# Optimization experiments

Measured on AMD Instinct MI355X. Metric: run time of the kernel, lower is better.

## Reference

```python
import math
import jax, jax.numpy as jnp
import numpy as np

B, T, N_FEAT, H = 16, 1024, 512, 8
D_K = N_FEAT // H  # 64


def setup_inputs() -> dict:
    key = jax.random.key(0)
    ks = jax.random.split(key, 16)
    s = 0.02
    return {
        "query": jax.random.normal(ks[0], (B, T, N_FEAT), jnp.float32),
        "key": jax.random.normal(ks[1], (B, T, N_FEAT), jnp.float32),
        "value": jax.random.normal(ks[2], (B, T, N_FEAT), jnp.float32),
        "pos_emb": jax.random.normal(ks[3], (1, T, N_FEAT), jnp.float32),
        "mask": jnp.zeros((B, 1, T), jnp.float32),  # additive bias, 0 = attend
        "Wq": jax.random.normal(ks[4], (N_FEAT, N_FEAT), jnp.float32) * s,
        "bq": jnp.zeros((N_FEAT,), jnp.float32),
        "Wk": jax.random.normal(ks[5], (N_FEAT, N_FEAT), jnp.float32) * s,
        "bk": jnp.zeros((N_FEAT,), jnp.float32),
        "Wv": jax.random.normal(ks[6], (N_FEAT, N_FEAT), jnp.float32) * s,
        "bv": jnp.zeros((N_FEAT,), jnp.float32),
        "Wo": jax.random.normal(ks[7], (N_FEAT, N_FEAT), jnp.float32) * s,
        "bo": jnp.zeros((N_FEAT,), jnp.float32),
        "Wpos": jax.random.normal(ks[8], (N_FEAT, N_FEAT), jnp.float32) * s,
        "pos_bias_u": jax.random.normal(ks[9], (H, D_K), jnp.float32) * 0.05,
        "pos_bias_v": jax.random.normal(ks[10], (H, D_K), jnp.float32) * 0.05,
    }


def reference(query, key, value, pos_emb, mask,
              Wq, bq, Wk, bk, Wv, bv, Wo, bo, Wpos,
              pos_bias_u, pos_bias_v):
    b, t, _ = query.shape
    h, d_k = pos_bias_u.shape
    # projections -> head-split
    q = (query @ Wq + bq).reshape(b, t, h, d_k)                 # (B,T,H,D)
    k = (key @ Wk + bk).reshape(b, -1, h, d_k).transpose(0, 2, 1, 3)    # (B,H,S,D)
    v = (value @ Wv + bv).reshape(b, -1, h, d_k).transpose(0, 2, 1, 3)  # (B,H,S,D)
    p = (pos_emb @ Wpos).reshape(pos_emb.shape[1], h, d_k).transpose(1, 0, 2)  # (H,S,D)
    # Transformer-XL content/position biased queries
    q_u = (q + pos_bias_u).transpose(0, 2, 1, 3)  # (B,H,T,D)
    q_v = (q + pos_bias_v).transpose(0, 2, 1, 3)  # (B,H,T,D)
    matrix_ac = jnp.einsum('bhtd,bhsd->bhts', q_u, k)
    matrix_bd = jnp.einsum('bhtd,hsd->bhts', q_v, p)
    scores = (matrix_ac + matrix_bd) / math.sqrt(d_k) + mask[:, None]  # (B,H,T,S)
    attn = jax.nn.softmax(scores, axis=-1)
    out = jnp.einsum('bhts,bhsd->bthd', attn, v).reshape(b, t, h * d_k)
    return out @ Wo + bo  # (B,T,n_feat)
```

## Files before the change

kernel.cpp:

```cpp
#include <hip/hip_runtime.h>

#define BB 16
#define TT 1024
#define HH 8
#define DD 64
#define NF 512

typedef __attribute__((ext_vector_type(4))) float f4;
typedef __attribute__((ext_vector_type(8))) short s8;
typedef __attribute__((ext_vector_type(2))) unsigned int u32x2;
typedef unsigned short u16;
typedef unsigned int u32;

#define LOG2E 1.4426950408889634f

__device__ __forceinline__ u16 f2bf(float x){
    unsigned int u = __builtin_bit_cast(unsigned int, x);
    u = (u + 0x7FFFu + ((u >> 16) & 1u)) >> 16;
    return (u16)u;
}
__device__ __forceinline__ float bf2f(u16 h){
    unsigned int u = ((unsigned int)h) << 16;
    return __builtin_bit_cast(float, u);
}
__device__ __forceinline__ u32 cvt_pk(float a, float b){
    u32 r; asm("v_cvt_pk_bf16_f32 %0, %1, %2" : "=v"(r) : "v"(a), "v"(b)); return r;
}
__device__ __forceinline__ float lo_bf(u32 p){ return __builtin_bit_cast(float, p << 16); }
__device__ __forceinline__ float hi_bf(u32 p){ return __builtin_bit_cast(float, p & 0xFFFF0000u); }

__global__ __launch_bounds__(256) void prep_w(const float* __restrict__ Wq,
    const float* __restrict__ Wk, const float* __restrict__ Wv,
    const float* __restrict__ Wpos, const float* __restrict__ Wo,
    u16* __restrict__ wtq, u16* __restrict__ wtk, u16* __restrict__ wtv,
    u16* __restrict__ wtp, u16* __restrict__ wohi, u16* __restrict__ wolo)
{
    __shared__ float tile[32][33];
    const int which = blockIdx.z;
    const float* W = which==0?Wq:which==1?Wk:which==2?Wv:which==3?Wpos:Wo;
    const int n0 = blockIdx.x*32, k0 = blockIdx.y*32;
    const int tc = threadIdx.x & 31, tr = threadIdx.x >> 5;
#pragma unroll
    for (int i=0;i<4;i++){ int r = tr + i*8; tile[r][tc] = W[(size_t)(k0+r)*NF + n0+tc]; }
    __syncthreads();
#pragma unroll
    for (int i=0;i<4;i++){
        int n = tr + i*8, k = tc;
        float val = tile[k][n];
        u16 hi = f2bf(val);
        size_t off = (size_t)(n0+n)*NF + k0+k;
        if (which==0) wtq[off]=hi; else if (which==1) wtk[off]=hi;
        else if (which==2) wtv[off]=hi; else if (which==3) wtp[off]=hi;
        else { wohi[off]=hi; wolo[off]=f2bf(val - bf2f(hi)); }
    }
}

template<int MODE>
__global__ __launch_bounds__(256) void gemm_bf16(const float* __restrict__ A,
                                                 const u16* __restrict__ Wt,
                                                 const float* __restrict__ bias,
                                                 const u16* __restrict__ padd,
                                                 const float* __restrict__ pbias,
                                                 u16* __restrict__ out)
{
    __shared__ __align__(16) u16 As[128*64];
    __shared__ __align__(16) u16 Bs[128*64];
    const int tid = threadIdx.x;
    const int row0 = blockIdx.x*128, col0 = blockIdx.y*128;
    const int wid = tid>>6, lane = tid&63, lm = lane&15, lg = lane>>4;
    const int wm = wid>>1, wn = wid&1;

    f4 acc[4][4];
#pragma unroll
    for (int i=0;i<4;i++)
#pragma unroll
        for (int j=0;j<4;j++) acc[i][j] = (f4){0.f,0.f,0.f,0.f};

    for (int k0=0;k0<NF;k0+=64){
        f4 areg[8]; s8 breg[4];
#pragma unroll
        for (int it=0; it<8; ++it){
            int idx = (it*256 + tid)*4;
            int m = idx>>6, k = idx&63;
            areg[it] = *(const f4*)(&A[(size_t)(row0+m)*NF + k0 + k]);
        }
#pragma unroll
        for (int it=0; it<4; ++it){
            int idx = (it*256 + tid)*8;
            int n = idx>>6, k = idx&63;
            breg[it] = *(const s8*)(&Wt[(size_t)(col0+n)*NF + k0 + k]);
        }
        __syncthreads();
#pragma unroll
        for (int it=0; it<8; ++it){
            int idx = (it*256+tid)*4;
            int m = idx>>6, k = idx&63;
            u32x2 pk;
            pk[0] = cvt_pk(areg[it][0], areg[it][1]);
            pk[1] = cvt_pk(areg[it][2], areg[it][3]);
            *(u32x2*)((char*)As + ((m*128 + k*2) ^ ((m&7)<<4))) = pk;
        }
#pragma unroll
        for (int it=0; it<4; ++it){
            int idx = (it*256+tid)*8;
            int n = idx>>6, k = idx&63;
            *(s8*)((char*)Bs + ((n*128 + k*2) ^ ((n&7)<<4))) = breg[it];
        }
        __syncthreads();
        s8 af[4][2], bf[4][2];
#pragma unroll
        for (int i=0;i<4;i++){
            int m = wm*64 + i*16 + lm;
#pragma unroll
            for (int c=0;c<2;c++)
                af[i][c] = *(const s8*)((char*)As + ((m*128 + c*64 + lg*16) ^ ((m&7)<<4)));
        }
#pragma unroll
        for (int j=0;j<4;j++){
            int n = wn*64 + j*16 + lm;
#pragma unroll
            for (int c=0;c<2;c++)
                bf[j][c] = *(const s8*)((char*)Bs + ((n*128 + c*64 + lg*16) ^ ((n&7)<<4)));
        }
#pragma unroll
        for (int i=0;i<4;i++)
#pragma unroll
            for (int j=0;j<4;j++)
#pragma unroll
                for (int c=0;c<2;c++)
                    acc[i][j] = __builtin_amdgcn_mfma_f32_16x16x32_bf16(af[i][c], bf[j][c], acc[i][j], 0,0,0);
    }

#pragma unroll
    for (int i=0;i<4;i++){
#pragma unroll
        for (int j=0;j<4;j++){
#pragma unroll
            for (int r=0;r<4;r++){
                const int m = row0 + wm*64 + i*16 + lg*4 + r;
                const int n = col0 + wn*64 + j*16 + lm;
                float val = acc[i][j][r];
                const int hh = n>>6, dd = n&63;
                if (MODE == 0){
                    out[(size_t)(hh*TT + m)*64 + dd] = f2bf(val);
                } else {
                    val += bias[n];
                    const int b_ = m>>10, t_ = m&1023;
                    if (MODE == 2) val += bf2f(padd[(size_t)(hh*TT + t_)*64 + dd]);
                    if (MODE == 5) val += pbias[n];
                    if (MODE == 3)
                        out[(((size_t)(b_*HH+hh))*DD + dd)*TT + t_] = f2bf(val);
                    else
                        out[((size_t)(b_*HH+hh)*TT + t_)*64 + dd] = f2bf(val);
                }
            }
        }
    }
}

__global__ __launch_bounds__(256) void gemm_final(const u16* __restrict__ Ahg,
    const u16* __restrict__ Alg,
    const u16* __restrict__ Bhg, const u16* __restrict__ Blg,
    const float* __restrict__ bias, float* __restrict__ out)
{
    __shared__ __align__(16) u16 Ah[128*64];
    __shared__ __align__(16) u16 Al[128*64];
    __shared__ __align__(16) u16 Bh[128*64];
    __shared__ __align__(16) u16 Bl[128*64];
    const int tid = threadIdx.x;
    const int row0 = blockIdx.x*128, col0 = blockIdx.y*128;
    const int wid = tid>>6, lane = tid&63, lm = lane&15, lg = lane>>4;
    const int wm = wid>>1, wn = wid&1;

    f4 acc[4][4];
#pragma unroll
    for (int i=0;i<4;i++)
#pragma unroll
        for (int j=0;j<4;j++) acc[i][j] = (f4){0.f,0.f,0.f,0.f};

    for (int k0=0;k0<NF;k0+=64){
        s8 ahreg[4], alreg[4], bhreg[4], blreg[4];
#pragma unroll
        for (int it=0; it<4; ++it){
            int idx = (it*256 + tid)*8;
            int m = idx>>6, k = idx&63;
            ahreg[it] = *(const s8*)(&Ahg[(size_t)(row0+m)*NF + k0 + k]);
            alreg[it] = *(const s8*)(&Alg[(size_t)(row0+m)*NF + k0 + k]);
            bhreg[it] = *(const s8*)(&Bhg[(size_t)(col0+m)*NF + k0 + k]);
            blreg[it] = *(const s8*)(&Blg[(size_t)(col0+m)*NF + k0 + k]);
        }
        __syncthreads();
#pragma unroll
        for (int it=0; it<4; ++it){
            int idx = (it*256+tid)*8;
            int m = idx>>6, k = idx&63;
            int off = (m*128 + k*2) ^ ((m&7)<<4);
            *(s8*)((char*)Ah + off) = ahreg[it];
            *(s8*)((char*)Al + off) = alreg[it];
            *(s8*)((char*)Bh + off) = bhreg[it];
            *(s8*)((char*)Bl + off) = blreg[it];
        }
        __syncthreads();
#pragma unroll
        for (int c=0;c<2;c++){
            s8 ah[4], al[4], bh4[4], bl4[4];
#pragma unroll
            for (int i=0;i<4;i++){
                int m = wm*64 + i*16 + lm;
                int off = (m*128 + c*64 + lg*16) ^ ((m&7)<<4);
                ah[i] = *(const s8*)((char*)Ah + off);
                al[i] = *(const s8*)((char*)Al + off);
            }
#pragma unroll
            for (int j=0;j<4;j++){
                int n = wn*64 + j*16 + lm;
                int off = (n*128 + c*64 + lg*16) ^ ((n&7)<<4);
                bh4[j] = *(const s8*)((char*)Bh + off);
                bl4[j] = *(const s8*)((char*)Bl + off);
            }
#pragma unroll
            for (int i=0;i<4;i++)
#pragma unroll
                for (int j=0;j<4;j++){
                    acc[i][j] = __builtin_amdgcn_mfma_f32_16x16x32_bf16(al[i], bh4[j], acc[i][j], 0,0,0);
                    acc[i][j] = __builtin_amdgcn_mfma_f32_16x16x32_bf16(ah[i], bl4[j], acc[i][j], 0,0,0);
                    acc[i][j] = __builtin_amdgcn_mfma_f32_16x16x32_bf16(ah[i], bh4[j], acc[i][j], 0,0,0);
                }
        }
    }

#pragma unroll
    for (int i=0;i<4;i++)
#pragma unroll
        for (int j=0;j<4;j++)
#pragma unroll
            for (int r=0;r<4;r++){
                const int m = row0 + wm*64 + i*16 + lg*4 + r;
                const int n = col0 + wn*64 + j*16 + lm;
                out[(size_t)m*NF + n] = acc[i][j][r] + bias[n];
            }
}

__global__ __launch_bounds__(256) void sbias2(const u16* __restrict__ p,
                                              const float* __restrict__ pbu,
                                              const float* __restrict__ pbv,
                                              const float* __restrict__ mask,
                                              float* __restrict__ sb)
{
    const int w    = blockIdx.x * 4 + (threadIdx.x >> 6);
    const int lane = threadIdx.x & 63;
    const int s = w & 1023;
    const int h = w >> 10;
    const float diff = pbv[h*64 + lane] - pbu[h*64 + lane];
    const float pv = bf2f(p[(size_t)(h*TT + s)*64 + lane]);
    float val = diff * pv;
#pragma unroll
    for (int off = 32; off; off >>= 1) val += __shfl_xor(val, off);
    if (lane < BB)
        sb[(size_t)(lane*HH + h)*TT + s] = (val * 0.125f + mask[lane*TT + s]) * LOG2E;
}

#define ATTN_GLOAD(tile) do { \
  _Pragma("unroll") for (int it=0; it<2; ++it){ \
    int idx = (it*256+tid)*8; int row_ = idx>>6, col_ = idx&63; \
    kh[it] = *(const s8*)(kb + (size_t)((tile)*64+row_)*64 + col_); \
    vh[it] = *(const s8*)(vtb + (size_t)row_*TT + (tile)*64 + col_); } } while(0)

#define ATTN_SSTORE(buf) do { \
  _Pragma("unroll") for (int it=0; it<2; ++it){ \
    int idx = (it*256+tid)*8; int row_ = idx>>6, col_ = idx&63; \
    int off_ = (row_*128 + col_*2) ^ ((row_&7)<<4); \
    *(s8*)((char*)Ks[(buf)] + off_) = kh[it]; \
    *(s8*)((char*)Vt[(buf)] + off_) = vh[it]; } } while(0)

#define ATTN_QK(buf, scv) do { \
  _Pragma("unroll") for (int j=0;j<4;j++){ \
    int srow_ = j*16+lm; \
    s8 kf0 = *(const s8*)((char*)Ks[(buf)] + ((srow_*128 + lg*16) ^ ((srow_&7)<<4))); \
    s8 kf1 = *(const s8*)((char*)Ks[(buf)] + ((srow_*128 + 64 + lg*16) ^ ((srow_&7)<<4))); \
    scv[j] = __builtin_amdgcn_mfma_f32_16x16x32_bf16(kf0, qf[0], scv[j], 0,0,0); \
    scv[j] = __builtin_amdgcn_mfma_f32_16x16x32_bf16(kf1, qf[1], scv[j], 0,0,0); } } while(0)

#define ATTN_STEP(i, CUR, SCUR, SNXT) do { \
    if ((i) < 15) ATTN_SSTORE((CUR)^1); \
    if ((i) < 14) ATTN_GLOAD((i)+2); \
    __syncthreads(); \
    f4 sbf[4]; \
    _Pragma("unroll") for (int j=0;j<4;j++) sbf[j] = *(const f4*)(sbb + (i)*64 + 16*j + 4*lg); \
    if ((i) < 15){ \
        _Pragma("unroll") for (int j=0;j<4;j++) SNXT[j] = (f4){0.f,0.f,0.f,0.f}; \
        __builtin_amdgcn_s_setprio(1); \
        ATTN_QK((CUR)^1, SNXT); \
        __builtin_amdgcn_s_setprio(0); \
    } \
    s8 vtf[4][2]; \
    _Pragma("unroll") for (int n=0;n<4;n++){ \
        int drow_ = n*16 + lm; \
        _Pragma("unroll") for (int c=0;c<2;c++) \
            vtf[n][c] = *(const s8*)((char*)Vt[(CUR)] + ((drow_*128 + c*64 + lg*16) ^ ((drow_&7)<<4))); \
    } \
    f4 p[4]; \
    _Pragma("unroll") for (int j=0;j<4;j++) \
        _Pragma("unroll") for (int r=0;r<4;r++) \
            p[j][r] = __builtin_exp2f(SCUR[j][r]*SCL + sbf[j][r]); \
    lsum4 += (p[0] + p[1]) + (p[2] + p[3]); \
    _Pragma("unroll") for (int j=0;j<4;j++){ \
        u32x2 w_; \
        w_[0] = cvt_pk(p[j][0], p[j][1]); \
        w_[1] = cvt_pk(p[j][2], p[j][3]); \
        *(u32x2*)((char*)Ps + ((prow*128 + (16*j + 4*lg)*2) ^ ((prow&7)<<4))) = w_; \
    } \
    s8 pf0 = *(const s8*)((char*)Ps + ((prow*128 +  0 + lg*16) ^ ((prow&7)<<4))); \
    s8 pf1 = *(const s8*)((char*)Ps + ((prow*128 + 64 + lg*16) ^ ((prow&7)<<4))); \
    __builtin_amdgcn_s_setprio(1); \
    _Pragma("unroll") for (int n=0;n<4;n++){ \
        oacc[n] = __builtin_amdgcn_mfma_f32_16x16x32_bf16(vtf[n][0], pf0, oacc[n], 0,0,0); \
        oacc[n] = __builtin_amdgcn_mfma_f32_16x16x32_bf16(vtf[n][1], pf1, oacc[n], 0,0,0); \
    } \
    __builtin_amdgcn_s_setprio(0); \
    __syncthreads(); \
} while(0)

__global__ __launch_bounds__(256,3) void attn8(const u16* __restrict__ q,
                                               const u16* __restrict__ kp,
                                               const u16* __restrict__ vt,
                                               const float* __restrict__ sb,
                                               u16* __restrict__ aoh,
                                               u16* __restrict__ aol)
{
    __shared__ __align__(16) u16 Ks[2][64*64];
    __shared__ __align__(16) u16 Vt[2][64*64];
    __shared__ __align__(16) u16 Ps[64*64];

    const int tid = threadIdx.x;
    const int wid = tid>>6, lane = tid&63, lm = lane&15, lg = lane>>4;
    const int bid = blockIdx.x;
    const int xcd = bid & 7, slot = bid >> 3;
    const int bh = xcd + 8*(slot >> 4);
    const int qt = slot & 15;
    const int t0 = qt*64;
    const int b = bh >> 3, h = bh & 7;
    const u16* qb  = q  + (size_t)bh*TT*64;
    const u16* kb  = kp + (size_t)bh*TT*64;
    const u16* vtb = vt + (size_t)bh*DD*TT;
    const float* sbb = sb + (size_t)bh*TT;

    s8 qf[2];
    qf[0] = *(const s8*)(qb + (size_t)(t0 + wid*16 + lm)*64 + lg*8);
    qf[1] = *(const s8*)(qb + (size_t)(t0 + wid*16 + lm)*64 + 32 + lg*8);

    f4 lsum4 = (f4){0.f,0.f,0.f,0.f};
    f4 oacc[4];
#pragma unroll
    for (int n=0;n<4;n++) oacc[n] = (f4){0.f,0.f,0.f,0.f};
    f4 scA[4], scB[4];

    const float SCL = 0.125f * LOG2E;
    const int prow = wid*16 + lm;

    s8 kh[2], vh[2];

    ATTN_GLOAD(0);
    ATTN_SSTORE(0);
    ATTN_GLOAD(1);
    __syncthreads();
#pragma unroll
    for (int j=0;j<4;j++) scA[j] = (f4){0.f,0.f,0.f,0.f};
    ATTN_QK(0, scA);

    for (int ii=0; ii<8; ++ii){
        ATTN_STEP(2*ii,   0, scA, scB);
        ATTN_STEP(2*ii+1, 1, scB, scA);
    }

    float ls = (lsum4[0]+lsum4[1]) + (lsum4[2]+lsum4[3]);
    ls += __shfl_xor(ls, 16);
    ls += __shfl_xor(ls, 32);
    const float inv = 1.f / ls;
    const size_t row = (size_t)(b*TT + t0 + wid*16 + lm)*NF + h*64;
#pragma unroll
    for (int n=0; n<4; ++n){
        f4 o = oacc[n] * inv;
        u32 h0 = cvt_pk(o[0], o[1]);
        u32 h1 = cvt_pk(o[2], o[3]);
        u32 l0 = cvt_pk(o[0]-lo_bf(h0), o[1]-hi_bf(h0));
        u32 l1 = cvt_pk(o[2]-lo_bf(h1), o[3]-hi_bf(h1));
        *(u32x2*)(&aoh[row + n*16 + lg*4]) = (u32x2){h0,h1};
        *(u32x2*)(&aol[row + n*16 + lg*4]) = (u32x2){l0,l1};
    }
}

extern "C" void kernel_launch(void* const* d_in, const int* in_sizes, int n_in,
                              void* d_out, int out_size, void* d_ws, size_t ws_size,
                              hipStream_t stream)
{
    const float* query   = (const float*)d_in[0];
    const float* key     = (const float*)d_in[1];
    const float* value   = (const float*)d_in[2];
    const float* pos_emb = (const float*)d_in[3];
    const float* mask    = (const float*)d_in[4];
    const float* Wq   = (const float*)d_in[5];
    const float* bq   = (const float*)d_in[6];
    const float* Wk   = (const float*)d_in[7];
    const float* bk   = (const float*)d_in[8];
    const float* Wv   = (const float*)d_in[9];
    const float* bv   = (const float*)d_in[10];
    const float* Wo   = (const float*)d_in[11];
    const float* bo   = (const float*)d_in[12];
    const float* Wpos = (const float*)d_in[13];
    const float* pbu  = (const float*)d_in[14];
    const float* pbv  = (const float*)d_in[15];
    float* out = (float*)d_out;

    char* ws = (char*)d_ws;
    size_t o = 0;
    u16* wtq  = (u16*)(ws + o); o += (size_t)NF*NF*2;
    u16* wtk  = (u16*)(ws + o); o += (size_t)NF*NF*2;
    u16* wtv  = (u16*)(ws + o); o += (size_t)NF*NF*2;
    u16* wtp  = (u16*)(ws + o); o += (size_t)NF*NF*2;
    u16* wohi = (u16*)(ws + o); o += (size_t)NF*NF*2;
    u16* wolo = (u16*)(ws + o); o += (size_t)NF*NF*2;
    u16* p_ws  = (u16*)(ws + o); o += (size_t)HH*TT*DD*2;
    u16* q_ws  = (u16*)(ws + o); o += (size_t)BB*HH*TT*DD*2;
    u16* kp_ws = (u16*)(ws + o); o += (size_t)BB*HH*TT*DD*2;
    u16* vt_ws = (u16*)(ws + o); o += (size_t)BB*HH*TT*DD*2;
    float* sb_ws = (float*)(ws + o); o += (size_t)BB*HH*TT*4;
    u16* aoh_ws = (u16*)(ws + o); o += (size_t)BB*TT*NF*2;
    u16* aol_ws = (u16*)(ws + o); o += (size_t)BB*TT*NF*2;

    const dim3 blk(256);

    prep_w<<<dim3(16,16,5), blk, 0, stream>>>(Wq, Wk, Wv, Wpos, Wo,
                                              wtq, wtk, wtv, wtp, wohi, wolo);
    gemm_bf16<0><<<dim3(TT/128, 4), blk, 0, stream>>>(pos_emb, wtp, nullptr, nullptr, nullptr, p_ws);
    sbias2<<<dim3(HH*TT/4), blk, 0, stream>>>(p_ws, pbu, pbv, mask, sb_ws);
    gemm_bf16<5><<<dim3(BB*TT/128, 4), blk, 0, stream>>>(query, wtq, bq, nullptr, pbu, q_ws);
    gemm_bf16<2><<<dim3(BB*TT/128, 4), blk, 0, stream>>>(key,   wtk, bk, p_ws, nullptr, kp_ws);
    gemm_bf16<3><<<dim3(BB*TT/128, 4), blk, 0, stream>>>(value, wtv, bv, nullptr, nullptr, vt_ws);
    attn8<<<dim3(BB*HH*TT/64), blk, 0, stream>>>(q_ws, kp_ws, vt_ws, sb_ws, aoh_ws, aol_ws);
    gemm_final<<<dim3(BB*TT/128, 4), blk, 0, stream>>>(aoh_ws, aol_ws, wohi, wolo, bo, out);
}
```

Measured before the change: 179.4 us.

## Load bf16 tiles directly to LDS and merge Q/K/V projections into one launch

Replaces the register-staged global-to-LDS copies of bf16 weight and activation tiles with global_load_lds direct transfers, using an XOR swizzle on the source address so the LDS layout matches the existing swizzled reads. The three separate Q, K, V projection launches become one grid with a z dimension that selects the input, weights and epilogue. The goals are lower VGPR pressure and instruction count in the load path, and less launch overhead and tail idle time across the projection GEMMs. The risk is that the direct-to-LDS layout must line up exactly with the swizzle the reads expect, and that the issued loads are not separately waited on before the barrier.

After: 203.8 us. +13.6%, slower.

```diff
diff --git a/kernel.cpp b/kernel.cpp
--- a/kernel.cpp
+++ b/kernel.cpp
@@ -28,6 +28,17 @@
 }
 __device__ __forceinline__ float lo_bf(u32 p){ return __builtin_bit_cast(float, p << 16); }
 __device__ __forceinline__ float hi_bf(u32 p){ return __builtin_bit_cast(float, p & 0xFFFF0000u); }
+
+#define GLOAD_TILE_SWZ(GPTR, LDSARR, ROW0) do { \
+  _Pragma("unroll") for (int it_=0; it_<4; ++it_){ \
+    int idx16_ = it_*256 + tid; \
+    int n_ = idx16_>>3; \
+    int kg_ = ((idx16_&7) ^ (n_&7))*8; \
+    const u16* g_ = &GPTR[(size_t)((ROW0)+n_)*NF + k0 + kg_]; \
+    __builtin_amdgcn_global_load_lds( \
+        (const __attribute__((address_space(1))) void*)g_, \
+        (__attribute__((address_space(3))) void*)&LDSARR[(it_*4+wid)*512], 16, 0, 0); \
+  } } while(0)
 
 __global__ __launch_bounds__(256) void prep_w(const float* __restrict__ Wq,
     const float* __restrict__ Wk, const float* __restrict__ Wv,
@@ -55,13 +66,9 @@
     }
 }
 
-template<int MODE>
-__global__ __launch_bounds__(256) void gemm_bf16(const float* __restrict__ A,
-                                                 const u16* __restrict__ Wt,
-                                                 const float* __restrict__ bias,
-                                                 const u16* __restrict__ padd,
-                                                 const float* __restrict__ pbias,
-                                                 u16* __restrict__ out)
+__global__ __launch_bounds__(256) void pos_gemm(const float* __restrict__ A,
+                                                const u16* __restrict__ Wt,
+                                                u16* __restrict__ out)
 {
     __shared__ __align__(16) u16 As[128*64];
     __shared__ __align__(16) u16 Bs[128*64];
@@ -77,20 +84,15 @@
         for (int j=0;j<4;j++) acc[i][j] = (f4){0.f,0.f,0.f,0.f};
 
     for (int k0=0;k0<NF;k0+=64){
-        f4 areg[8]; s8 breg[4];
+        f4 areg[8];
 #pragma unroll
         for (int it=0; it<8; ++it){
             int idx = (it*256 + tid)*4;
             int m = idx>>6, k = idx&63;
             areg[it] = *(const f4*)(&A[(size_t)(row0+m)*NF + k0 + k]);
         }
-#pragma unroll
-        for (int it=0; it<4; ++it){
-            int idx = (it*256 + tid)*8;
-            int n = idx>>6, k = idx&63;
-            breg[it] = *(const s8*)(&Wt[(size_t)(col0+n)*NF + k0 + k]);
-        }
         __syncthreads();
+        GLOAD_TILE_SWZ(Wt, Bs, col0);
 #pragma unroll
         for (int it=0; it<8; ++it){
             int idx = (it*256+tid)*4;
@@ -100,12 +102,6 @@
             pk[1] = cvt_pk(areg[it][2], areg[it][3]);
             *(u32x2*)((char*)As + ((m*128 + k*2) ^ ((m&7)<<4))) = pk;
         }
-#pragma unroll
-        for (int it=0; it<4; ++it){
-            int idx = (it*256+tid)*8;
-            int n = idx>>6, k = idx&63;
-            *(s8*)((char*)Bs + ((n*128 + k*2) ^ ((n&7)<<4))) = breg[it];
-        }
         __syncthreads();
         s8 af[4][2], bf[4][2];
 #pragma unroll
@@ -132,26 +128,105 @@
     }
 
 #pragma unroll
-    for (int i=0;i<4;i++){
-#pragma unroll
-        for (int j=0;j<4;j++){
+    for (int i=0;i<4;i++)
+#pragma unroll
+        for (int j=0;j<4;j++)
 #pragma unroll
             for (int r=0;r<4;r++){
                 const int m = row0 + wm*64 + i*16 + lg*4 + r;
                 const int n = col0 + wn*64 + j*16 + lm;
-                float val = acc[i][j][r];
                 const int hh = n>>6, dd = n&63;
-                if (MODE == 0){
-                    out[(size_t)(hh*TT + m)*64 + dd] = f2bf(val);
+                out[(size_t)(hh*TT + m)*64 + dd] = f2bf(acc[i][j][r]);
+            }
+}
+
+__global__ __launch_bounds__(256) void qkv_gemm(
+    const float* __restrict__ Aq, const float* __restrict__ Ak, const float* __restrict__ Av,
+    const u16* __restrict__ Wtq, const u16* __restrict__ Wtk, const u16* __restrict__ Wtv,
+    const float* __restrict__ bq, const float* __restrict__ bk, const float* __restrict__ bv,
+    const u16* __restrict__ padd, const float* __restrict__ pbu,
+    u16* __restrict__ oq, u16* __restrict__ okp, u16* __restrict__ ovt)
+{
+    __shared__ __align__(16) u16 As[128*64];
+    __shared__ __align__(16) u16 Bs[128*64];
+    const int tid = threadIdx.x;
+    const int z = blockIdx.z;
+    const float* A    = z==0?Aq : z==1?Ak : Av;
+    const u16*   Wt   = z==0?Wtq: z==1?Wtk: Wtv;
+    const float* bias = z==0?bq : z==1?bk : bv;
+    const int row0 = blockIdx.x*128, col0 = blockIdx.y*128;
+    const int wid = tid>>6, lane = tid&63, lm = lane&15, lg = lane>>4;
+    const int wm = wid>>1, wn = wid&1;
+
+    f4 acc[4][4];
+#pragma unroll
+    for (int i=0;i<4;i++)
+#pragma unroll
+        for (int j=0;j<4;j++) acc[i][j] = (f4){0.f,0.f,0.f,0.f};
+
+    for (int k0=0;k0<NF;k0+=64){
+        f4 areg[8];
+#pragma unroll
+        for (int it=0; it<8; ++it){
+            int idx = (it*256 + tid)*4;
+            int m = idx>>6, k = idx&63;
+            areg[it] = *(const f4*)(&A[(size_t)(row0+m)*NF + k0 + k]);
+        }
+        __syncthreads();
+        GLOAD_TILE_SWZ(Wt, Bs, col0);
+#pragma unroll
+        for (int it=0; it<8; ++it){
+            int idx = (it*256+tid)*4;
+            int m = idx>>6, k = idx&63;
+            u32x2 pk;
+            pk[0] = cvt_pk(areg[it][0], areg[it][1]);
+            pk[1] = cvt_pk(areg[it][2], areg[it][3]);
+            *(u32x2*)((char*)As + ((m*128 + k*2) ^ ((m&7)<<4))) = pk;
+        }
+        __syncthreads();
+        s8 af[4][2], bf[4][2];
+#pragma unroll
+        for (int i=0;i<4;i++){
+            int m = wm*64 + i*16 + lm;
+#pragma unroll
+            for (int c=0;c<2;c++)
+                af[i][c] = *(const s8*)((char*)As + ((m*128 + c*64 + lg*16) ^ ((m&7)<<4)));
+        }
+#pragma unroll
+        for (int j=0;j<4;j++){
+            int n = wn*64 + j*16 + lm;
+#pragma unroll
+            for (int c=0;c<2;c++)
+                bf[j][c] = *(const s8*)((char*)Bs + ((n*128 + c*64 + lg*16) ^ ((n&7)<<4)));
+        }
+#pragma unroll
+        for (int i=0;i<4;i++)
+#pragma unroll
+            for (int j=0;j<4;j++)
+#pragma unroll
+                for (int c=0;c<2;c++)
+                    acc[i][j] = __builtin_amdgcn_mfma_f32_16x16x32_bf16(af[i][c], bf[j][c], acc[i][j], 0,0,0);
+    }
+
+#pragma unroll
+    for (int i=0;i<4;i++){
+#pragma unroll
+        for (int j=0;j<4;j++){
+#pragma unroll
+            for (int r=0;r<4;r++){
+                const int m = row0 + wm*64 + i*16 + lg*4 + r;
+                const int n = col0 + wn*64 + j*16 + lm;
+                float val = acc[i][j][r] + bias[n];
+                const int hh = n>>6, dd = n&63;
+                const int b_ = m>>10, t_ = m&1023;
+                if (z == 0){
+                    val += pbu[n];
+                    oq[((size_t)(b_*HH+hh)*TT + t_)*64 + dd] = f2bf(val);
+                } else if (z == 1){
+                    val += bf2f(padd[(size_t)(hh*TT + t_)*64 + dd]);
+                    okp[((size_t)(b_*HH+hh)*TT + t_)*64 + dd] = f2bf(val);
                 } else {
-                    val += bias[n];
-                    const int b_ = m>>10, t_ = m&1023;
-                    if (MODE == 2) val += bf2f(padd[(size_t)(hh*TT + t_)*64 + dd]);
-                    if (MODE == 5) val += pbias[n];
-                    if (MODE == 3)
-                        out[(((size_t)(b_*HH+hh))*DD + dd)*TT + t_] = f2bf(val);
-                    else
-                        out[((size_t)(b_*HH+hh)*TT + t_)*64 + dd] = f2bf(val);
+                    ovt[(((size_t)(b_*HH+hh))*DD + dd)*TT + t_] = f2bf(val);
                 }
             }
         }
@@ -179,27 +254,11 @@
         for (int j=0;j<4;j++) acc[i][j] = (f4){0.f,0.f,0.f,0.f};
 
     for (int k0=0;k0<NF;k0+=64){
-        s8 ahreg[4], alreg[4], bhreg[4], blreg[4];
-#pragma unroll
-        for (int it=0; it<4; ++it){
-            int idx = (it*256 + tid)*8;
-            int m = idx>>6, k = idx&63;
-            ahreg[it] = *(const s8*)(&Ahg[(size_t)(row0+m)*NF + k0 + k]);
-            alreg[it] = *(const s8*)(&Alg[(size_t)(row0+m)*NF + k0 + k]);
-            bhreg[it] = *(const s8*)(&Bhg[(size_t)(col0+m)*NF + k0 + k]);
-            blreg[it] = *(const s8*)(&Blg[(size_t)(col0+m)*NF + k0 + k]);
-        }
         __syncthreads();
-#pragma unroll
-        for (int it=0; it<4; ++it){
-            int idx = (it*256+tid)*8;
-            int m = idx>>6, k = idx&63;
-            int off = (m*128 + k*2) ^ ((m&7)<<4);
-            *(s8*)((char*)Ah + off) = ahreg[it];
-            *(s8*)((char*)Al + off) = alreg[it];
-            *(s8*)((char*)Bh + off) = bhreg[it];
-            *(s8*)((char*)Bl + off) = blreg[it];
-        }
+        GLOAD_TILE_SWZ(Ahg, Ah, row0);
+        GLOAD_TILE_SWZ(Alg, Al, row0);
+        GLOAD_TILE_SWZ(Bhg, Bh, col0);
+        GLOAD_TILE_SWZ(Blg, Bl, col0);
         __syncthreads();
 #pragma unroll
         for (int c=0;c<2;c++){
@@ -432,11 +491,11 @@
 
     prep_w<<<dim3(16,16,5), blk, 0, stream>>>(Wq, Wk, Wv, Wpos, Wo,
                                               wtq, wtk, wtv, wtp, wohi, wolo);
-    gemm_bf16<0><<<dim3(TT/128, 4), blk, 0, stream>>>(pos_emb, wtp, nullptr, nullptr, nullptr, p_ws);
+    pos_gemm<<<dim3(TT/128, 4), blk, 0, stream>>>(pos_emb, wtp, p_ws);
     sbias2<<<dim3(HH*TT/4), blk, 0, stream>>>(p_ws, pbu, pbv, mask, sb_ws);
-    gemm_bf16<5><<<dim3(BB*TT/128, 4), blk, 0, stream>>>(query, wtq, bq, nullptr, pbu, q_ws);
-    gemm_bf16<2><<<dim3(BB*TT/128, 4), blk, 0, stream>>>(key,   wtk, bk, p_ws, nullptr, kp_ws);
-    gemm_bf16<3><<<dim3(BB*TT/128, 4), blk, 0, stream>>>(value, wtv, bv, nullptr, nullptr, vt_ws);
+    qkv_gemm<<<dim3(BB*TT/128, 4, 3), blk, 0, stream>>>(
+        query, key, value, wtq, wtk, wtv, bq, bk, bv, p_ws, pbu,
+        q_ws, kp_ws, vt_ws);
     attn8<<<dim3(BB*HH*TT/64), blk, 0, stream>>>(q_ws, kp_ws, vt_ws, sb_ws, aoh_ws, aol_ws);
     gemm_final<<<dim3(BB*TT/128, 4), blk, 0, stream>>>(aoh_ws, aol_ws, wohi, wolo, bo, out);
 }
```

## Process 128 query rows per attention block with two row groups per wave

Applied to the files above, without the earlier changes.

The attention kernel now handles 128 query rows per block, two 16-row groups per wave, so each K/V tile loaded into shared memory is reused twice as much and the grid is halved. In exchange it drops the software pipelining that computed the next tile's QK scores ahead of the softmax/PV stage, so QK now runs in-step. It also roughly doubles per-wave accumulator registers, which may hurt occupancy under launch_bounds(256,3), and doubles the P scratch buffer in shared memory.

New measurement: 311.4 us. 1.74x slower.

```diff
diff --git a/kernel.cpp b/kernel.cpp
--- a/kernel.cpp
+++ b/kernel.cpp
@@ -273,90 +273,98 @@
     *(s8*)((char*)Ks[(buf)] + off_) = kh[it]; \
     *(s8*)((char*)Vt[(buf)] + off_) = vh[it]; } } while(0)
 
-#define ATTN_QK(buf, scv) do { \
-  _Pragma("unroll") for (int j=0;j<4;j++){ \
-    int srow_ = j*16+lm; \
-    s8 kf0 = *(const s8*)((char*)Ks[(buf)] + ((srow_*128 + lg*16) ^ ((srow_&7)<<4))); \
-    s8 kf1 = *(const s8*)((char*)Ks[(buf)] + ((srow_*128 + 64 + lg*16) ^ ((srow_&7)<<4))); \
-    scv[j] = __builtin_amdgcn_mfma_f32_16x16x32_bf16(kf0, qf[0], scv[j], 0,0,0); \
-    scv[j] = __builtin_amdgcn_mfma_f32_16x16x32_bf16(kf1, qf[1], scv[j], 0,0,0); } } while(0)
-
-#define ATTN_STEP(i, CUR, SCUR, SNXT) do { \
+#define ATTN_STEP(i, CUR) do { \
     if ((i) < 15) ATTN_SSTORE((CUR)^1); \
     if ((i) < 14) ATTN_GLOAD((i)+2); \
     __syncthreads(); \
     f4 sbf[4]; \
     _Pragma("unroll") for (int j=0;j<4;j++) sbf[j] = *(const f4*)(sbb + (i)*64 + 16*j + 4*lg); \
-    if ((i) < 15){ \
-        _Pragma("unroll") for (int j=0;j<4;j++) SNXT[j] = (f4){0.f,0.f,0.f,0.f}; \
-        __builtin_amdgcn_s_setprio(1); \
-        ATTN_QK((CUR)^1, SNXT); \
-        __builtin_amdgcn_s_setprio(0); \
+    f4 sc[2][4]; \
+    _Pragma("unroll") for (int g=0;g<2;g++) \
+        _Pragma("unroll") for (int j=0;j<4;j++) sc[g][j] = (f4){0.f,0.f,0.f,0.f}; \
+    __builtin_amdgcn_s_setprio(1); \
+    _Pragma("unroll") for (int j=0;j<4;j++){ \
+        int srow_ = j*16+lm; \
+        s8 kf0 = *(const s8*)((char*)Ks[(CUR)] + ((srow_*128 + lg*16) ^ ((srow_&7)<<4))); \
+        s8 kf1 = *(const s8*)((char*)Ks[(CUR)] + ((srow_*128 + 64 + lg*16) ^ ((srow_&7)<<4))); \
+        sc[0][j] = __builtin_amdgcn_mfma_f32_16x16x32_bf16(kf0, qf[0][0], sc[0][j], 0,0,0); \
+        sc[0][j] = __builtin_amdgcn_mfma_f32_16x16x32_bf16(kf1, qf[0][1], sc[0][j], 0,0,0); \
+        sc[1][j] = __builtin_amdgcn_mfma_f32_16x16x32_bf16(kf0, qf[1][0], sc[1][j], 0,0,0); \
+        sc[1][j] = __builtin_amdgcn_mfma_f32_16x16x32_bf16(kf1, qf[1][1], sc[1][j], 0,0,0); \
     } \
+    __builtin_amdgcn_s_setprio(0); \
     s8 vtf[4][2]; \
     _Pragma("unroll") for (int n=0;n<4;n++){ \
         int drow_ = n*16 + lm; \
         _Pragma("unroll") for (int c=0;c<2;c++) \
             vtf[n][c] = *(const s8*)((char*)Vt[(CUR)] + ((drow_*128 + c*64 + lg*16) ^ ((drow_&7)<<4))); \
     } \
-    f4 p[4]; \
-    _Pragma("unroll") for (int j=0;j<4;j++) \
-        _Pragma("unroll") for (int r=0;r<4;r++) \
-            p[j][r] = __builtin_exp2f(SCUR[j][r]*SCL + sbf[j][r]); \
-    lsum4 += (p[0] + p[1]) + (p[2] + p[3]); \
-    _Pragma("unroll") for (int j=0;j<4;j++){ \
-        u32x2 w_; \
-        w_[0] = cvt_pk(p[j][0], p[j][1]); \
-        w_[1] = cvt_pk(p[j][2], p[j][3]); \
-        *(u32x2*)((char*)Ps + ((prow*128 + (16*j + 4*lg)*2) ^ ((prow&7)<<4))) = w_; \
+    _Pragma("unroll") for (int g=0; g<2; ++g){ \
+        const int prow = wid*32 + g*16 + lm; \
+        f4 p[4]; \
+        _Pragma("unroll") for (int j=0;j<4;j++) \
+            _Pragma("unroll") for (int r=0;r<4;r++) \
+                p[j][r] = __builtin_exp2f(sc[g][j][r]*SCL + sbf[j][r]); \
+        lsum4[g] += (p[0] + p[1]) + (p[2] + p[3]); \
+        _Pragma("unroll") for (int j=0;j<4;j++){ \
+            u32x2 w_; \
+            w_[0] = cvt_pk(p[j][0], p[j][1]); \
+            w_[1] = cvt_pk(p[j][2], p[j][3]); \
+            *(u32x2*)((char*)Ps + ((prow*128 + (16*j + 4*lg)*2) ^ ((prow&7)<<4))) = w_; \
+        } \
+        s8 pf0 = *(const s8*)((char*)Ps + ((prow*128 +  0 + lg*16) ^ ((prow&7)<<4))); \
+        s8 pf1 = *(const s8*)((char*)Ps + ((prow*128 + 64 + lg*16) ^ ((prow&7)<<4))); \
+        __builtin_amdgcn_s_setprio(1); \
+        _Pragma("unroll") for (int n=0;n<4;n++){ \
+            oacc[g][n] = __builtin_amdgcn_mfma_f32_16x16x32_bf16(vtf[n][0], pf0, oacc[g][n], 0,0,0); \
+            oacc[g][n] = __builtin_amdgcn_mfma_f32_16x16x32_bf16(vtf[n][1], pf1, oacc[g][n], 0,0,0); \
+        } \
+        __builtin_amdgcn_s_setprio(0); \
     } \
-    s8 pf0 = *(const s8*)((char*)Ps + ((prow*128 +  0 + lg*16) ^ ((prow&7)<<4))); \
-    s8 pf1 = *(const s8*)((char*)Ps + ((prow*128 + 64 + lg*16) ^ ((prow&7)<<4))); \
-    __builtin_amdgcn_s_setprio(1); \
-    _Pragma("unroll") for (int n=0;n<4;n++){ \
-        oacc[n] = __builtin_amdgcn_mfma_f32_16x16x32_bf16(vtf[n][0], pf0, oacc[n], 0,0,0); \
-        oacc[n] = __builtin_amdgcn_mfma_f32_16x16x32_bf16(vtf[n][1], pf1, oacc[n], 0,0,0); \
-    } \
-    __builtin_amdgcn_s_setprio(0); \
     __syncthreads(); \
 } while(0)
 
-__global__ __launch_bounds__(256,3) void attn8(const u16* __restrict__ q,
-                                               const u16* __restrict__ kp,
-                                               const u16* __restrict__ vt,
-                                               const float* __restrict__ sb,
-                                               u16* __restrict__ aoh,
-                                               u16* __restrict__ aol)
+__global__ __launch_bounds__(256,3) void attn10(const u16* __restrict__ q,
+                                                const u16* __restrict__ kp,
+                                                const u16* __restrict__ vt,
+                                                const float* __restrict__ sb,
+                                                u16* __restrict__ aoh,
+                                                u16* __restrict__ aol)
 {
     __shared__ __align__(16) u16 Ks[2][64*64];
     __shared__ __align__(16) u16 Vt[2][64*64];
-    __shared__ __align__(16) u16 Ps[64*64];
+    __shared__ __align__(16) u16 Ps[128*64];
 
     const int tid = threadIdx.x;
     const int wid = tid>>6, lane = tid&63, lm = lane&15, lg = lane>>4;
     const int bid = blockIdx.x;
     const int xcd = bid & 7, slot = bid >> 3;
-    const int bh = xcd + 8*(slot >> 4);
-    const int qt = slot & 15;
-    const int t0 = qt*64;
+    const int bh = xcd + 8*(slot >> 3);
+    const int qt = slot & 7;
+    const int t0 = qt*128;
     const int b = bh >> 3, h = bh & 7;
     const u16* qb  = q  + (size_t)bh*TT*64;
     const u16* kb  = kp + (size_t)bh*TT*64;
     const u16* vtb = vt + (size_t)bh*DD*TT;
     const float* sbb = sb + (size_t)bh*TT;
 
-    s8 qf[2];
-    qf[0] = *(const s8*)(qb + (size_t)(t0 + wid*16 + lm)*64 + lg*8);
-    qf[1] = *(const s8*)(qb + (size_t)(t0 + wid*16 + lm)*64 + 32 + lg*8);
-
-    f4 lsum4 = (f4){0.f,0.f,0.f,0.f};
-    f4 oacc[4];
-#pragma unroll
-    for (int n=0;n<4;n++) oacc[n] = (f4){0.f,0.f,0.f,0.f};
-    f4 scA[4], scB[4];
+    s8 qf[2][2];
+#pragma unroll
+    for (int g=0; g<2; ++g)
+#pragma unroll
+        for (int c=0; c<2; ++c)
+            qf[g][c] = *(const s8*)(qb + (size_t)(t0 + wid*32 + g*16 + lm)*64 + 32*c + lg*8);
+
+    f4 lsum4[2];
+    lsum4[0] = (f4){0.f,0.f,0.f,0.f};
+    lsum4[1] = (f4){0.f,0.f,0.f,0.f};
+    f4 oacc[2][4];
+#pragma unroll
+    for (int g=0;g<2;g++)
+#pragma unroll
+        for (int n=0;n<4;n++) oacc[g][n] = (f4){0.f,0.f,0.f,0.f};
 
     const float SCL = 0.125f * LOG2E;
-    const int prow = wid*16 + lm;
 
     s8 kh[2], vh[2];
 
@@ -364,29 +372,29 @@
     ATTN_SSTORE(0);
     ATTN_GLOAD(1);
     __syncthreads();
-#pragma unroll
-    for (int j=0;j<4;j++) scA[j] = (f4){0.f,0.f,0.f,0.f};
-    ATTN_QK(0, scA);
 
     for (int ii=0; ii<8; ++ii){
-        ATTN_STEP(2*ii,   0, scA, scB);
-        ATTN_STEP(2*ii+1, 1, scB, scA);
-    }
-
-    float ls = (lsum4[0]+lsum4[1]) + (lsum4[2]+lsum4[3]);
-    ls += __shfl_xor(ls, 16);
-    ls += __shfl_xor(ls, 32);
-    const float inv = 1.f / ls;
-    const size_t row = (size_t)(b*TT + t0 + wid*16 + lm)*NF + h*64;
-#pragma unroll
-    for (int n=0; n<4; ++n){
-        f4 o = oacc[n] * inv;
-        u32 h0 = cvt_pk(o[0], o[1]);
-        u32 h1 = cvt_pk(o[2], o[3]);
-        u32 l0 = cvt_pk(o[0]-lo_bf(h0), o[1]-hi_bf(h0));
-        u32 l1 = cvt_pk(o[2]-lo_bf(h1), o[3]-hi_bf(h1));
-        *(u32x2*)(&aoh[row + n*16 + lg*4]) = (u32x2){h0,h1};
-        *(u32x2*)(&aol[row + n*16 + lg*4]) = (u32x2){l0,l1};
+        ATTN_STEP(2*ii,   0);
+        ATTN_STEP(2*ii+1, 1);
+    }
+
+#pragma unroll
+    for (int g=0; g<2; ++g){
+        float ls = (lsum4[g][0]+lsum4[g][1]) + (lsum4[g][2]+lsum4[g][3]);
+        ls += __shfl_xor(ls, 16);
+        ls += __shfl_xor(ls, 32);
+        const float inv = 1.f / ls;
+        const size_t row = (size_t)(b*TT + t0 + wid*32 + g*16 + lm)*NF + h*64;
+#pragma unroll
+        for (int n=0; n<4; ++n){
+            f4 o = oacc[g][n] * inv;
+            u32 h0 = cvt_pk(o[0], o[1]);
+            u32 h1 = cvt_pk(o[2], o[3]);
+            u32 l0 = cvt_pk(o[0]-lo_bf(h0), o[1]-hi_bf(h0));
+            u32 l1 = cvt_pk(o[2]-lo_bf(h1), o[3]-hi_bf(h1));
+            *(u32x2*)(&aoh[row + n*16 + lg*4]) = (u32x2){h0,h1};
+            *(u32x2*)(&aol[row + n*16 + lg*4]) = (u32x2){l0,l1};
+        }
     }
 }
 
@@ -437,6 +445,6 @@
     gemm_bf16<5><<<dim3(BB*TT/128, 4), blk, 0, stream>>>(query, wtq, bq, nullptr, pbu, q_ws);
     gemm_bf16<2><<<dim3(BB*TT/128, 4), blk, 0, stream>>>(key,   wtk, bk, p_ws, nullptr, kp_ws);
     gemm_bf16<3><<<dim3(BB*TT/128, 4), blk, 0, stream>>>(value, wtv, bv, nullptr, nullptr, vt_ws);
-    attn8<<<dim3(BB*HH*TT/64), blk, 0, stream>>>(q_ws, kp_ws, vt_ws, sb_ws, aoh_ws, aol_ws);
+    attn10<<<dim3(BB*HH*TT/128), blk, 0, stream>>>(q_ws, kp_ws, vt_ws, sb_ws, aoh_ws, aol_ws);
     gemm_final<<<dim3(BB*TT/128, 4), blk, 0, stream>>>(aoh_ws, aol_ws, wohi, wolo, bo, out);
 }
```
